# Performance work log

Hardware: AMD Instinct MI355X
Metric: run time of the kernel (lower is better)

Reference implementation:

```python
import jax, jax.numpy as jnp
import numpy as np
from jax import lax

# --- Haar (db1) wavelet filters, per WTConv (dec filters use reversed pywt taps) ---
_R = 0.7071067811865476
_lo = jnp.array([_R, _R], jnp.float32)
_hi = jnp.array([_R, -_R], jnp.float32)
# order: LL, (hi rows)x(lo cols), (lo rows)x(hi cols), HH  — matches WTConv stack order
DEC = jnp.stack([_lo[:, None] * _lo[None, :], _hi[:, None] * _lo[None, :],
                 _lo[:, None] * _hi[None, :], _hi[:, None] * _hi[None, :]])  # [4,2,2]
REC = DEC  # Haar is orthogonal: rec filters equal dec filters


def dwconv(x, w):
    # depthwise conv, SAME padding; x [b,c,h,w], w [c,1,kh,kw]
    return lax.conv_general_dilated(x, w, (1, 1), 'SAME',
                                    feature_group_count=x.shape[1],
                                    dimension_numbers=('NCHW', 'OIHW', 'NCHW'))


def wtconv(x, base_w, base_s, wav_w, wav_s):
    # WTConv2d, wt_levels=1, Haar: base depthwise path + wavelet-domain depthwise conv path
    b, c, h, w = x.shape
    # analysis: stride-2 2x2 filters == non-overlapping block contraction
    s = jnp.einsum('bchpwq,fpq->bcfhw', x.reshape(b, c, h // 2, 2, w // 2, 2), DEC)
    s = s.reshape(b, 4 * c, h // 2, w // 2)
    s = dwconv(s, wav_w) * wav_s[None, :, None, None]  # conv subbands + scale (init 0.1)
    # synthesis: transposed stride-2 conv == block expansion
    y = jnp.einsum('bcfhw,fpq->bchpwq', s.reshape(b, c, 4, h // 2, w // 2), REC)
    y = y.reshape(b, c, h, w)
    return dwconv(x, base_w) * base_s[None, :, None, None] + y


def _forward(x, crossFeat, Wq, Wk, Wv, temperature,
             qdw_base_w, qdw_base_s, qdw_wav_w, qdw_wav_s,
             kdw_base_w, kdw_base_s, kdw_wav_w, kdw_wav_s,
             vdw_base_w, vdw_base_s, vdw_wav_w, vdw_wav_s,
             proj_base_w, proj_base_s, proj_wav_w, proj_wav_s):
    heads = temperature.shape[0]
    b, _, H, W = crossFeat.shape
    q = jnp.einsum('bchw,oc->bohw', x, Wq)          # 1x1 conv, bias=False
    k = jnp.einsum('bchw,oc->bohw', crossFeat, Wk)
    v = jnp.einsum('bchw,oc->bohw', crossFeat, Wv)
    q = wtconv(q, qdw_base_w, qdw_base_s, qdw_wav_w, qdw_wav_s)
    k = wtconv(k, kdw_base_w, kdw_base_s, kdw_wav_w, kdw_wav_s)
    v = wtconv(v, vdw_base_w, vdw_base_s, vdw_wav_w, vdw_wav_s)
    dim = q.shape[1]
    # F.interpolate(mode='bilinear', align_corners=False) == jax.image.resize 'bilinear'
    q = jax.image.resize(q, (b, dim, H, W), 'bilinear')
    ch = dim // heads
    q = q.reshape(b, heads, ch, H * W)
    k = k.reshape(b, heads, ch, H * W)
    v = v.reshape(b, heads, ch, H * W)
    # L2-normalize along spatial dim (torch F.normalize eps=1e-12)
    q = q / jnp.maximum(jnp.linalg.norm(q, axis=-1, keepdims=True), 1e-12)
    k = k / jnp.maximum(jnp.linalg.norm(k, axis=-1, keepdims=True), 1e-12)
    attn = jnp.einsum('bhcn,bhdn->bhcd', q, k) * temperature[None]  # [b,h,ch,ch]
    attn = jax.nn.softmax(attn, axis=-1)
    out = jnp.einsum('bhcd,bhdn->bhcn', attn, v).reshape(b, dim, H, W)
    return wtconv(out, proj_base_w, proj_base_s, proj_wav_w, proj_wav_s)


def setup_inputs() -> dict:
    key = jax.random.key(0)
    ks = iter(jax.random.split(key, 32))
    B, CIN, DIM, HEADS = 2, 256, 256, 8
    d = {}
    d['x'] = jax.random.normal(next(ks), (B, CIN, 64, 64), jnp.float32)
    d['crossFeat'] = jax.random.normal(next(ks), (B, CIN, 128, 128), jnp.float32)
    d['Wq'] = jax.random.normal(next(ks), (DIM, CIN), jnp.float32) * 0.05
    d['Wk'] = jax.random.normal(next(ks), (DIM, CIN), jnp.float32) * 0.05
    d['Wv'] = jax.random.normal(next(ks), (DIM, CIN), jnp.float32) * 0.05
    d['temperature'] = jnp.ones((HEADS, 1, 1), jnp.float32)
    for pre, ksz in [('qdw', 3), ('kdw', 3), ('vdw', 3), ('proj', 1)]:
        d[pre + '_base_w'] = jax.random.normal(next(ks), (DIM, 1, ksz, ksz), jnp.float32) * 0.1
        d[pre + '_base_s'] = jnp.ones((DIM,), jnp.float32)
        d[pre + '_wav_w'] = jax.random.normal(next(ks), (4 * DIM, 1, ksz, ksz), jnp.float32) * 0.1
        d[pre + '_wav_s'] = 0.1 * jnp.ones((4 * DIM,), jnp.float32)
    return d


def reference(x, crossFeat, Wq, Wk, Wv, temperature,
              qdw_base_w, qdw_base_s, qdw_wav_w, qdw_wav_s,
              kdw_base_w, kdw_base_s, kdw_wav_w, kdw_wav_s,
              vdw_base_w, vdw_base_s, vdw_wav_w, vdw_wav_s,
              proj_base_w, proj_base_s, proj_wav_w, proj_wav_s):
    return _forward(x, crossFeat, Wq, Wk, Wv, temperature,
                    qdw_base_w, qdw_base_s, qdw_wav_w, qdw_wav_s,
                    kdw_base_w, kdw_base_s, kdw_wav_w, kdw_wav_s,
                    vdw_base_w, vdw_base_s, vdw_wav_w, vdw_wav_s,
                    proj_base_w, proj_base_s, proj_wav_w, proj_wav_s)
```

## Files before the change

### kernel.cpp

```cpp
#include <hip/hip_runtime.h>
#include <math.h>

constexpr int B_ = 2;
constexpr int C_ = 256;
constexpr int Hb_ = 128, Wb_ = 128;
constexpr int Nb_ = Hb_ * Wb_;
constexpr int Hs_ = 64, Ws_ = 64;
constexpr int Ns_ = Hs_ * Ws_;
constexpr int HEADS_ = 8;
constexpr int CHD_ = C_ / HEADS_;

typedef float f32x4 __attribute__((ext_vector_type(4)));
typedef short bf16x8 __attribute__((ext_vector_type(8)));
typedef unsigned short u16x8 __attribute__((ext_vector_type(8)));

__device__ inline void cvt_split(float f, unsigned short& h, unsigned short& l) {
  unsigned u = __float_as_uint(f);
  unsigned r = u + 0x7fffu + ((u >> 16) & 1u);
  h = (unsigned short)(r >> 16);
  float hf = __uint_as_float((unsigned)h << 16);
  float lo = f - hf;
  unsigned u2 = __float_as_uint(lo);
  unsigned r2 = u2 + 0x7fffu + ((u2 >> 16) & 1u);
  l = (unsigned short)(r2 >> 16);
}

__global__ __launch_bounds__(256) void cvt_split_T(const float* __restrict__ X,
                                                   unsigned short* __restrict__ Xh,
                                                   unsigned short* __restrict__ Xl,
                                                   int NTOT) {
  __shared__ float xs[64][72];
  const int b  = blockIdx.z;
  const int c0 = blockIdx.y * 64;
  const int n0 = blockIdx.x * 64;
  const int t  = threadIdx.x;
  const float* xb = X + ((size_t)(b * C_ + c0)) * NTOT + n0;
  {
    int cl = t >> 4, n4 = (t & 15) << 2;
#pragma unroll
    for (int i = 0; i < 4; ++i) {
      float4 v = *(const float4*)(xb + (size_t)(cl + 16 * i) * NTOT + n4);
      *(float4*)&xs[cl + 16 * i][n4] = v;
    }
  }
  __syncthreads();
  const int n_l = t >> 2, cqb = t & 3;
  size_t obase = ((size_t)b * NTOT + n0 + n_l) * C_ + c0;
#pragma unroll
  for (int it = 0; it < 2; ++it) {
    int cq = it * 4 + cqb;
    u16x8 hv, lv;
#pragma unroll
    for (int j = 0; j < 8; ++j) {
      unsigned short h, l;
      cvt_split(xs[cq * 8 + j][n_l], h, l);
      hv[j] = h; lv[j] = l;
    }
    *(u16x8*)(Xh + obase + cq * 8) = hv;
    *(u16x8*)(Xl + obase + cq * 8) = lv;
  }
}

__global__ void cvt_w(const float* __restrict__ Wq, const float* __restrict__ Wk,
                      const float* __restrict__ Wv, unsigned short* __restrict__ Wp) {
  int i = blockIdx.x * 256 + threadIdx.x;
  int m = i >> 16, idx = i & 65535;
  const float* src = (m == 0) ? Wq : (m == 1) ? Wk : Wv;
  unsigned short h, l;
  cvt_split(src[idx], h, l);
  Wp[(size_t)m * 131072 + idx] = h;
  Wp[(size_t)m * 131072 + 65536 + idx] = l;
}

template<bool DUAL>
__global__ __launch_bounds__(256) void gemm_mfma(
    const unsigned short* __restrict__ XhT, const unsigned short* __restrict__ XlT,
    const unsigned short* __restrict__ Wh1, const unsigned short* __restrict__ Wl1,
    const unsigned short* __restrict__ Wh2, const unsigned short* __restrict__ Wl2,
    float* __restrict__ out1, float* __restrict__ out2, int NTOT) {
  __shared__ __align__(16) unsigned short XhL[64][40];
  __shared__ __align__(16) unsigned short XlL[64][40];
  const int b  = blockIdx.z;
  const int o0 = blockIdx.y * 64;
  const int n0 = blockIdx.x * 64;
  const int t  = threadIdx.x;
  const int w = t >> 6, lane = t & 63;
  const int lr = lane & 15, lk = lane >> 4;
  const unsigned short* xh = XhT + ((size_t)b * NTOT + n0) * C_;
  const unsigned short* xl = XlT + ((size_t)b * NTOT + n0) * C_;
  const int arow = o0 + w * 16 + lr;
  f32x4 acc1[4] = {};
  f32x4 acc2[4] = {};
  const int sn = t >> 2, scq = (t & 3) << 3;
  for (int c0 = 0; c0 < C_; c0 += 32) {
    {
      size_t off = (size_t)sn * C_ + c0 + scq;
      *(u16x8*)&XhL[sn][scq] = *(const u16x8*)(xh + off);
      *(u16x8*)&XlL[sn][scq] = *(const u16x8*)(xl + off);
    }
    size_t aoff = (size_t)arow * C_ + c0 + lk * 8;
    bf16x8 a1h = *(const bf16x8*)(Wh1 + aoff);
    bf16x8 a1l = *(const bf16x8*)(Wl1 + aoff);
    bf16x8 a2h, a2l;
    if constexpr (DUAL) {
      a2h = *(const bf16x8*)(Wh2 + aoff);
      a2l = *(const bf16x8*)(Wl2 + aoff);
    }
    __syncthreads();
#pragma unroll
    for (int s = 0; s < 4; ++s) {
      bf16x8 bh = *(const bf16x8*)&XhL[s * 16 + lr][lk * 8];
      bf16x8 bl = *(const bf16x8*)&XlL[s * 16 + lr][lk * 8];
      acc1[s] = __builtin_amdgcn_mfma_f32_16x16x32_bf16(a1h, bh, acc1[s], 0, 0, 0);
      acc1[s] = __builtin_amdgcn_mfma_f32_16x16x32_bf16(a1h, bl, acc1[s], 0, 0, 0);
      acc1[s] = __builtin_amdgcn_mfma_f32_16x16x32_bf16(a1l, bh, acc1[s], 0, 0, 0);
      if constexpr (DUAL) {
        acc2[s] = __builtin_amdgcn_mfma_f32_16x16x32_bf16(a2h, bh, acc2[s], 0, 0, 0);
        acc2[s] = __builtin_amdgcn_mfma_f32_16x16x32_bf16(a2h, bl, acc2[s], 0, 0, 0);
        acc2[s] = __builtin_amdgcn_mfma_f32_16x16x32_bf16(a2l, bh, acc2[s], 0, 0, 0);
      }
    }
    __syncthreads();
  }
  float* o1 = out1 + ((size_t)(b * C_ + o0 + w * 16)) * NTOT + n0;
#pragma unroll
  for (int s = 0; s < 4; ++s)
#pragma unroll
    for (int r = 0; r < 4; ++r)
      o1[(size_t)(lk * 4 + r) * NTOT + s * 16 + lr] = acc1[s][r];
  if constexpr (DUAL) {
    float* o2 = out2 + ((size_t)(b * C_ + o0 + w * 16)) * NTOT + n0;
#pragma unroll
    for (int s = 0; s < 4; ++s)
#pragma unroll
      for (int r = 0; r < 4; ++r)
        o2[(size_t)(lk * 4 + r) * NTOT + s * 16 + lr] = acc2[s][r];
  }
}

template<int HP>
__global__ __launch_bounds__(256) void wtconv_fused(
    const float* __restrict__ x, const float* __restrict__ bw,
    const float* __restrict__ bs, const float* __restrict__ ww,
    const float* __restrict__ wsc, float* __restrict__ out,
    float* __restrict__ nrm) {
  constexpr int NT = HP / 64;
  const int tile = blockIdx.x;
  const int c = blockIdx.y, b = blockIdx.z;
  const int oy = (tile / NT) * 64, ox = (tile % NT) * 64;
  const float* xp = x + ((size_t)(b * C_) + c) * HP * HP;

  __shared__ float xt[68][76];
  __shared__ f32x4 sb4[34][36];
  __shared__ float red[4];

  float wb[9];
#pragma unroll
  for (int i = 0; i < 9; ++i) wb[i] = bw[c * 9 + i];
  const float sbase = bs[c];
  f32x4 wv4[9]; f32x4 sv4;
#pragma unroll
  for (int i = 0; i < 9; ++i) {
    wv4[i].x = ww[(c * 4 + 0) * 9 + i];
    wv4[i].y = ww[(c * 4 + 1) * 9 + i];
    wv4[i].z = ww[(c * 4 + 2) * 9 + i];
    wv4[i].w = ww[(c * 4 + 3) * 9 + i];
  }
  sv4.x = wsc[c * 4 + 0]; sv4.y = wsc[c * 4 + 1];
  sv4.z = wsc[c * 4 + 2]; sv4.w = wsc[c * 4 + 3];

  const int t = threadIdx.x;
  for (int p = t; p < 68 * 18; p += 256) {
    int r = p / 18, k4 = (p % 18) << 2;
    int gy = oy - 2 + r, gx = ox - 4 + k4;
    float4 v = make_float4(0.f, 0.f, 0.f, 0.f);
    if ((unsigned)gy < (unsigned)HP && (unsigned)gx < (unsigned)HP)
      v = *(const float4*)(xp + (size_t)gy * HP + gx);
    *(float4*)&xt[r][k4] = v;
  }
  __syncthreads();
  for (int p = t; p < 34 * 34; p += 256) {
    int i = p / 34, j = p % 34;
    float p00 = xt[2 * i][2 * j + 2],     p01 = xt[2 * i][2 * j + 3];
    float p10 = xt[2 * i + 1][2 * j + 2], p11 = xt[2 * i + 1][2 * j + 3];
    f32x4 s;
    s.x = 0.5f * (p00 + p01 + p10 + p11);
    s.y = 0.5f * (p00 + p01 - p10 - p11);
    s.z = 0.5f * (p00 - p01 + p10 - p11);
    s.w = 0.5f * (p00 - p01 - p10 + p11);
    sb4[i][j] = s;
  }
  __syncthreads();

  float nacc = 0.f;
  float* op0 = out + ((size_t)(b * C_) + c) * HP * HP;
  for (int p = t; p < 32 * 32; p += 256) {
    int i = p >> 5, j = p & 31;
    f32x4 a4 = {0.f, 0.f, 0.f, 0.f};
#pragma unroll
    for (int dh = 0; dh < 3; ++dh)
#pragma unroll
      for (int dw = 0; dw < 3; ++dw)
        a4 += sb4[i + dh][j + dw] * wv4[dh * 3 + dw];
    f32x4 s4 = a4 * sv4;
    float pp[4][4];
#pragma unroll
    for (int r = 0; r < 4; ++r)
#pragma unroll
      for (int cc = 0; cc < 4; ++cc)
        pp[r][cc] = xt[2 * i + 1 + r][2 * j + 3 + cc];
    float o4[2][2];
#pragma unroll
    for (int di = 0; di < 2; ++di)
#pragma unroll
      for (int dj = 0; dj < 2; ++dj) {
        float a = 0.f;
#pragma unroll
        for (int dh = 0; dh < 3; ++dh)
#pragma unroll
          for (int dw = 0; dw < 3; ++dw)
            a = fmaf(pp[di + dh][dj + dw], wb[dh * 3 + dw], a);
        a *= sbase;
        float s1 = di ? -s4.y : s4.y;
        float s2 = dj ? -s4.z : s4.z;
        float s3 = (di ^ dj) ? -s4.w : s4.w;
        o4[di][dj] = a + 0.5f * (s4.x + s1 + s2 + s3);
      }
    float* op = op0 + (size_t)(oy + 2 * i) * HP + ox + 2 * j;
    *(float2*)op        = make_float2(o4[0][0], o4[0][1]);
    *(float2*)(op + HP) = make_float2(o4[1][0], o4[1][1]);
    nacc += o4[0][0] * o4[0][0] + o4[0][1] * o4[0][1] +
            o4[1][0] * o4[1][0] + o4[1][1] * o4[1][1];
  }
  if (nrm != nullptr) {
#pragma unroll
    for (int m = 32; m; m >>= 1) nacc += __shfl_xor(nacc, m, 64);
    int lane = t & 63, wv_ = t >> 6;
    if (lane == 0) red[wv_] = nacc;
    __syncthreads();
    if (t == 0)
      atomicAdd(&nrm[b * C_ + c], red[0] + red[1] + red[2] + red[3]);
  }
}

__global__ __launch_bounds__(256) void resize2x_norm(const float* __restrict__ in,
                                                     float* __restrict__ out,
                                                     float* __restrict__ rnq_sum) {
  const int bc = blockIdx.x;
  const int t = threadIdx.x;
  __shared__ float xs[64][65];
  __shared__ float red[4];
  const float* ip = in + (size_t)bc * Ns_;
  for (int p = t; p < 1024; p += 256) {
    float4 v = *(const float4*)&ip[p << 2];
    int r = p >> 4, c0 = (p & 15) << 2;
    xs[r][c0] = v.x; xs[r][c0 + 1] = v.y; xs[r][c0 + 2] = v.z; xs[r][c0 + 3] = v.w;
  }
  __syncthreads();
  float* op = out + (size_t)bc * Nb_;
  float nacc = 0.f;
#pragma unroll
  for (int it = 0; it < 16; ++it) {
    int p = t + it * 256;
    int i = p >> 5;
    int jc = p & 31;
    int ti = i >> 1; bool oi = i & 1;
    int r0 = oi ? ti : (ti > 0 ? ti - 1 : 0);
    int r1 = oi ? (ti < 63 ? ti + 1 : 63) : ti;
    float wr0 = oi ? 0.75f : 0.25f, wr1 = oi ? 0.25f : 0.75f;
    int cb = jc << 1;
    int cm1 = cb > 0 ? cb - 1 : 0;
    int cp2 = cb < 62 ? cb + 2 : 63;
    float a0 = xs[r0][cm1], a1 = xs[r0][cb], a2 = xs[r0][cb + 1], a3 = xs[r0][cp2];
    float b0 = xs[r1][cm1], b1 = xs[r1][cb], b2 = xs[r1][cb + 1], b3 = xs[r1][cp2];
    float ha0 = 0.25f * a0 + 0.75f * a1, hb0 = 0.25f * b0 + 0.75f * b1;
    float ha1 = 0.75f * a1 + 0.25f * a2, hb1 = 0.75f * b1 + 0.25f * b2;
    float ha2 = 0.25f * a1 + 0.75f * a2, hb2 = 0.25f * b1 + 0.75f * b2;
    float ha3 = 0.75f * a2 + 0.25f * a3, hb3 = 0.75f * b2 + 0.25f * b3;
    float4 o = make_float4(wr0 * ha0 + wr1 * hb0, wr0 * ha1 + wr1 * hb1,
                           wr0 * ha2 + wr1 * hb2, wr0 * ha3 + wr1 * hb3);
    *(float4*)&op[p << 2] = o;
    nacc += o.x * o.x + o.y * o.y + o.z * o.z + o.w * o.w;
  }
#pragma unroll
  for (int m = 32; m; m >>= 1) nacc += __shfl_xor(nacc, m, 64);
  int lane = t & 63, wv = t >> 6;
  if (lane == 0) red[wv] = nacc;
  __syncthreads();
  if (t == 0) rnq_sum[bc] = red[0] + red[1] + red[2] + red[3];
}

__global__ void zero_buf(float* __restrict__ p, int n) {
  int i = blockIdx.x * blockDim.x + threadIdx.x;
  if (i < n) p[i] = 0.f;
}

__global__ __launch_bounds__(256) void gram_qk(const float* __restrict__ q,
                                               const float* __restrict__ k,
                                               float* __restrict__ gram) {
  const int b = blockIdx.z, h = blockIdx.y, sl = blockIdx.x;
  constexpr int NS = Nb_ / 32;
  const int n0 = sl * NS;
  const int t = threadIdx.x;
  const int tc = t >> 4, td = t & 15;
  const float* qb = q + ((size_t)b * C_ + h * CHD_) * Nb_;
  const float* kb = k + ((size_t)b * C_ + h * CHD_) * Nb_;
  __shared__ float qs[32][132];
  __shared__ float kst[128][34];
  float a00 = 0.f, a01 = 0.f, a10 = 0.f, a11 = 0.f;
  for (int nc = 0; nc < NS; nc += 128) {
    for (int i = t; i < 1024; i += 256) {
      int row = i >> 5, nc4 = (i & 31) << 2;
      float4 qv = *(const float4*)&qb[(size_t)row * Nb_ + n0 + nc + nc4];
      *(float4*)&qs[row][nc4] = qv;
      float4 kv = *(const float4*)&kb[(size_t)row * Nb_ + n0 + nc + nc4];
      kst[nc4 + 0][row] = kv.x; kst[nc4 + 1][row] = kv.y;
      kst[nc4 + 2][row] = kv.z; kst[nc4 + 3][row] = kv.w;
    }
    __syncthreads();
#pragma unroll 8
    for (int nn = 0; nn < 128; ++nn) {
      float q0 = qs[2 * tc][nn], q1 = qs[2 * tc + 1][nn];
      float2 kk = *(float2*)&kst[nn][2 * td];
      a00 = fmaf(q0, kk.x, a00); a01 = fmaf(q0, kk.y, a01);
      a10 = fmaf(q1, kk.x, a10); a11 = fmaf(q1, kk.y, a11);
    }
    __syncthreads();
  }
  float* gp = gram + ((size_t)(b * HEADS_ + h) * CHD_ + 2 * tc) * CHD_ + 2 * td;
  atomicAdd(&gp[0], a00);
  atomicAdd(&gp[1], a01);
  atomicAdd(&gp[CHD_], a10);
  atomicAdd(&gp[CHD_ + 1], a11);
}

__global__ __launch_bounds__(1024) void attn_softmax(const float* __restrict__ gram,
                                                     const float* __restrict__ rnq_sum,
                                                     const float* __restrict__ rnk_sum,
                                                     const float* __restrict__ temp,
                                                     float* __restrict__ attn) {
  const int h = blockIdx.x, b = blockIdx.y;
  const int t = threadIdx.x;
  const int c = t >> 5, d = t & 31;
  size_t gi = ((size_t)(b * HEADS_ + h) * CHD_ + c) * CHD_ + d;
  float rq = 1.f / fmaxf(sqrtf(rnq_sum[b * C_ + h * CHD_ + c]), 1e-12f);
  float rk = 1.f / fmaxf(sqrtf(rnk_sum[b * C_ + h * CHD_ + d]), 1e-12f);
  float val = gram[gi] * rq * rk * temp[h];
  float m = val;
#pragma unroll
  for (int s = 16; s; s >>= 1) m = fmaxf(m, __shfl_xor(m, s, 64));
  float e = expf(val - m);
  float ssum = e;
#pragma unroll
  for (int s = 16; s; s >>= 1) ssum += __shfl_xor(ssum, s, 64);
  attn[gi] = e / ssum;
}

__global__ __launch_bounds__(256) void av_proj(const float* __restrict__ attn,
                                               const float* __restrict__ v,
                                               const float* __restrict__ p_bw,
                                               const float* __restrict__ p_bs,
                                               const float* __restrict__ p_ww,
                                               const float* __restrict__ p_ws,
                                               float* __restrict__ out) {
  const int bh = blockIdx.y;
  const int b = bh >> 3, h = bh & 7;
  const int half = threadIdx.x >> 7;
  const int pl = threadIdx.x & 127;
  const int p = blockIdx.x * 128 + pl;
  const int bi = p >> 6, bj = p & 63;
  __shared__ float at[32][36];
  for (int i = threadIdx.x; i < 1024; i += 256)
    at[i & 31][i >> 5] = attn[(size_t)bh * 1024 + i];
  __syncthreads();
  const float* vb = v + ((size_t)b * C_ + h * CHD_) * Nb_;
  const int n00 = (2 * bi) * Wb_ + 2 * bj;
  float acc[16][4] = {};
  for (int d = 0; d < 32; ++d) {
    const float* vp = vb + (size_t)d * Nb_ + n00;
    float2 vt = *(const float2*)vp;
    float2 vbt = *(const float2*)(vp + Wb_);
    float4 a0 = *(float4*)&at[d][half * 16];
    float4 a1 = *(float4*)&at[d][half * 16 + 4];
    float4 a2 = *(float4*)&at[d][half * 16 + 8];
    float4 a3 = *(float4*)&at[d][half * 16 + 12];
    float av[16] = {a0.x, a0.y, a0.z, a0.w, a1.x, a1.y, a1.z, a1.w,
                    a2.x, a2.y, a2.z, a2.w, a3.x, a3.y, a3.z, a3.w};
#pragma unroll
    for (int cc = 0; cc < 16; ++cc) {
      acc[cc][0] = fmaf(av[cc], vt.x,  acc[cc][0]);
      acc[cc][1] = fmaf(av[cc], vt.y,  acc[cc][1]);
      acc[cc][2] = fmaf(av[cc], vbt.x, acc[cc][2]);
      acc[cc][3] = fmaf(av[cc], vbt.y, acc[cc][3]);
    }
  }
  float* ob = out + ((size_t)b * C_ + h * CHD_) * Nb_;
#pragma unroll
  for (int cc = 0; cc < 16; ++cc) {
    int lc = half * 16 + cc;
    int gc = h * CHD_ + lc;
    float p00 = acc[cc][0], p01 = acc[cc][1], p10 = acc[cc][2], p11 = acc[cc][3];
    float ll = 0.5f * (p00 + p01 + p10 + p11) * (p_ww[gc * 4 + 0] * p_ws[gc * 4 + 0]);
    float hl = 0.5f * (p00 + p01 - p10 - p11) * (p_ww[gc * 4 + 1] * p_ws[gc * 4 + 1]);
    float lh = 0.5f * (p00 - p01 + p10 - p11) * (p_ww[gc * 4 + 2] * p_ws[gc * 4 + 2]);
    float hh = 0.5f * (p00 - p01 - p10 + p11) * (p_ww[gc * 4 + 3] * p_ws[gc * 4 + 3]);
    float bb = p_bw[gc] * p_bs[gc];
    float* op = ob + (size_t)lc * Nb_ + n00;
    *(float2*)op         = make_float2(p00 * bb + 0.5f * (ll + hl + lh + hh),
                                       p01 * bb + 0.5f * (ll + hl - lh - hh));
    *(float2*)(op + Wb_) = make_float2(p10 * bb + 0.5f * (ll - hl + lh - hh),
                                       p11 * bb + 0.5f * (ll - hl - lh + hh));
  }
}

extern "C" void kernel_launch(void* const* d_in, const int* in_sizes, int n_in,
                              void* d_out, int out_size, void* d_ws, size_t ws_size,
                              hipStream_t stream) {
  const float* x    = (const float*)d_in[0];
  const float* cf   = (const float*)d_in[1];
  const float* Wq   = (const float*)d_in[2];
  const float* Wk   = (const float*)d_in[3];
  const float* Wv   = (const float*)d_in[4];
  const float* temp = (const float*)d_in[5];
  const float* q_bw = (const float*)d_in[6];
  const float* q_bs = (const float*)d_in[7];
  const float* q_ww = (const float*)d_in[8];
  const float* q_ws = (const float*)d_in[9];
  const float* k_bw = (const float*)d_in[10];
  const float* k_bs = (const float*)d_in[11];
  const float* k_ww = (const float*)d_in[12];
  const float* k_ws = (const float*)d_in[13];
  const float* v_bw = (const float*)d_in[14];
  const float* v_bs = (const float*)d_in[15];
  const float* v_ww = (const float*)d_in[16];
  const float* v_ws = (const float*)d_in[17];
  const float* p_bw = (const float*)d_in[18];
  const float* p_bs = (const float*)d_in[19];
  const float* p_ww = (const float*)d_in[20];
  const float* p_ws = (const float*)d_in[21];

  float* ws   = (float*)d_ws;
  float* A    = ws;
  float* Bb   = A  + 2097152;
  float* Cb   = Bb + 8388608;
  float* Fb   = Cb + 8388608;
  float* Gb   = Fb + 2097152;
  float* Hb   = Gb + 8388608;
  float* XhKf = Hb + 8388608;
  float* XlKf = XhKf + 4194304;
  float* Xhxf = XlKf + 4194304;
  float* Xlxf = Xhxf + 1048576;
  float* Wpf  = Xlxf + 1048576;
  float* rnq  = Wpf + 196608;
  float* rnk  = rnq + 512;
  float* gram = rnk + 512;
  float* attn = gram + 16384;
  unsigned short* XhK = (unsigned short*)XhKf;
  unsigned short* XlK = (unsigned short*)XlKf;
  unsigned short* Xhx = (unsigned short*)Xhxf;
  unsigned short* Xlx = (unsigned short*)Xlxf;
  unsigned short* Wp  = (unsigned short*)Wpf;

  zero_buf<<<(16896 + 255) / 256, 256, 0, stream>>>(rnk, 16896);

  cvt_split_T<<<dim3(Nb_ / 64, C_ / 64, B_), 256, 0, stream>>>(cf, XhK, XlK, Nb_);
  cvt_split_T<<<dim3(Ns_ / 64, C_ / 64, B_), 256, 0, stream>>>(x,  Xhx, Xlx, Ns_);
  cvt_w<<<3 * 65536 / 256, 256, 0, stream>>>(Wq, Wk, Wv, Wp);

  gemm_mfma<false><<<dim3(Ns_ / 64, C_ / 64, B_), 256, 0, stream>>>(
      Xhx, Xlx, Wp, Wp + 65536, nullptr, nullptr, A, nullptr, Ns_);
  gemm_mfma<true><<<dim3(Nb_ / 64, C_ / 64, B_), 256, 0, stream>>>(
      XhK, XlK, Wp + 131072, Wp + 196608, Wp + 262144, Wp + 327680, Bb, Cb, Nb_);

  wtconv_fused<64><<<dim3(1, C_, B_), 256, 0, stream>>>(A, q_bw, q_bs, q_ww, q_ws, Fb, nullptr);
  wtconv_fused<128><<<dim3(4, C_, B_), 256, 0, stream>>>(Bb, k_bw, k_bs, k_ww, k_ws, Gb, rnk);
  wtconv_fused<128><<<dim3(4, C_, B_), 256, 0, stream>>>(Cb, v_bw, v_bs, v_ww, v_ws, Hb, nullptr);

  resize2x_norm<<<B_ * C_, 256, 0, stream>>>(Fb, Bb, rnq);

  gram_qk<<<dim3(32, HEADS_, B_), 256, 0, stream>>>(Bb, Gb, gram);
  attn_softmax<<<dim3(HEADS_, B_), 1024, 0, stream>>>(gram, rnq, rnk, temp, attn);

  av_proj<<<dim3(Nb_ / 4 / 128, B_ * HEADS_), 256, 0, stream>>>(
      attn, Hb, p_bw, p_bs, p_ww, p_ws, (float*)d_out);
}
```

Baseline: 286.6 us.

## Double-buffer GEMM tiles with register prefetch and widen N tile to 128

The split-bf16 MFMA projection GEMM now uses a 128-column N tile instead of 64 and double-buffers the X tiles in shared memory. Global loads for the next K-step are issued into registers before the current step's MFMAs, which removes one barrier per iteration and hides load latency. Weight fragments are also prefetched one step ahead. In exchange the kernel uses more accumulator registers and shared memory, and half as many blocks are launched, which may lower occupancy. The shared layout loses its padding, so LDS bank conflicts are possible.

```diff
diff --git a/kernel.cpp b/kernel.cpp
--- a/kernel.cpp
+++ b/kernel.cpp
@@ -78,39 +78,56 @@
     const unsigned short* __restrict__ Wh1, const unsigned short* __restrict__ Wl1,
     const unsigned short* __restrict__ Wh2, const unsigned short* __restrict__ Wl2,
     float* __restrict__ out1, float* __restrict__ out2, int NTOT) {
-  __shared__ __align__(16) unsigned short XhL[64][40];
-  __shared__ __align__(16) unsigned short XlL[64][40];
+  __shared__ __align__(16) unsigned short XhL[2][128 * 32];
+  __shared__ __align__(16) unsigned short XlL[2][128 * 32];
   const int b  = blockIdx.z;
   const int o0 = blockIdx.y * 64;
-  const int n0 = blockIdx.x * 64;
+  const int n0 = blockIdx.x * 128;
   const int t  = threadIdx.x;
   const int w = t >> 6, lane = t & 63;
   const int lr = lane & 15, lk = lane >> 4;
   const unsigned short* xh = XhT + ((size_t)b * NTOT + n0) * C_;
   const unsigned short* xl = XlT + ((size_t)b * NTOT + n0) * C_;
   const int arow = o0 + w * 16 + lr;
-  f32x4 acc1[4] = {};
-  f32x4 acc2[4] = {};
-  const int sn = t >> 2, scq = (t & 3) << 3;
-  for (int c0 = 0; c0 < C_; c0 += 32) {
-    {
-      size_t off = (size_t)sn * C_ + c0 + scq;
-      *(u16x8*)&XhL[sn][scq] = *(const u16x8*)(xh + off);
-      *(u16x8*)&XlL[sn][scq] = *(const u16x8*)(xl + off);
-    }
-    size_t aoff = (size_t)arow * C_ + c0 + lk * 8;
-    bf16x8 a1h = *(const bf16x8*)(Wh1 + aoff);
-    bf16x8 a1l = *(const bf16x8*)(Wl1 + aoff);
-    bf16x8 a2h, a2l;
-    if constexpr (DUAL) {
-      a2h = *(const bf16x8*)(Wh2 + aoff);
-      a2l = *(const bf16x8*)(Wl2 + aoff);
-    }
-    __syncthreads();
-#pragma unroll
-    for (int s = 0; s < 4; ++s) {
-      bf16x8 bh = *(const bf16x8*)&XhL[s * 16 + lr][lk * 8];
-      bf16x8 bl = *(const bf16x8*)&XlL[s * 16 + lr][lk * 8];
+  const size_t abase = (size_t)arow * C_ + lk * 8;
+  const size_t g0 = (size_t)(t >> 2) * C_ + (size_t)(t & 3) * 8;
+  const size_t g1 = (size_t)((t >> 2) + 64) * C_ + (size_t)(t & 3) * 8;
+  f32x4 acc1[8] = {};
+  f32x4 acc2[8] = {};
+  *(u16x8*)&XhL[0][t * 8]         = *(const u16x8*)(xh + g0);
+  *(u16x8*)&XhL[0][(t + 256) * 8] = *(const u16x8*)(xh + g1);
+  *(u16x8*)&XlL[0][t * 8]         = *(const u16x8*)(xl + g0);
+  *(u16x8*)&XlL[0][(t + 256) * 8] = *(const u16x8*)(xl + g1);
+  bf16x8 a1h = *(const bf16x8*)(Wh1 + abase);
+  bf16x8 a1l = *(const bf16x8*)(Wl1 + abase);
+  bf16x8 a2h = {}, a2l = {};
+  if constexpr (DUAL) {
+    a2h = *(const bf16x8*)(Wh2 + abase);
+    a2l = *(const bf16x8*)(Wl2 + abase);
+  }
+  __syncthreads();
+  for (int step = 0; step < 8; ++step) {
+    const int cur = step & 1;
+    u16x8 xr0h, xr1h, xr0l, xr1l;
+    bf16x8 n1h = {}, n1l = {}, n2h = {}, n2l = {};
+    const int c1 = (step + 1) * 32;
+    if (step < 7) {
+      xr0h = *(const u16x8*)(xh + g0 + c1);
+      xr1h = *(const u16x8*)(xh + g1 + c1);
+      xr0l = *(const u16x8*)(xl + g0 + c1);
+      xr1l = *(const u16x8*)(xl + g1 + c1);
+      n1h = *(const bf16x8*)(Wh1 + abase + c1);
+      n1l = *(const bf16x8*)(Wl1 + abase + c1);
+      if constexpr (DUAL) {
+        n2h = *(const bf16x8*)(Wh2 + abase + c1);
+        n2l = *(const bf16x8*)(Wl2 + abase + c1);
+      }
+    }
+#pragma unroll
+    for (int s = 0; s < 8; ++s) {
+      const int bo = ((s * 16 + lr) * 4 + lk) * 8;
+      bf16x8 bh = *(const bf16x8*)&XhL[cur][bo];
+      bf16x8 bl = *(const bf16x8*)&XlL[cur][bo];
       acc1[s] = __builtin_amdgcn_mfma_f32_16x16x32_bf16(a1h, bh, acc1[s], 0, 0, 0);
       acc1[s] = __builtin_amdgcn_mfma_f32_16x16x32_bf16(a1h, bl, acc1[s], 0, 0, 0);
       acc1[s] = __builtin_amdgcn_mfma_f32_16x16x32_bf16(a1l, bh, acc1[s], 0, 0, 0);
@@ -120,18 +137,27 @@
         acc2[s] = __builtin_amdgcn_mfma_f32_16x16x32_bf16(a2l, bh, acc2[s], 0, 0, 0);
       }
     }
+    if (step < 7) {
+      const int nxt = cur ^ 1;
+      *(u16x8*)&XhL[nxt][t * 8]         = xr0h;
+      *(u16x8*)&XhL[nxt][(t + 256) * 8] = xr1h;
+      *(u16x8*)&XlL[nxt][t * 8]         = xr0l;
+      *(u16x8*)&XlL[nxt][(t + 256) * 8] = xr1l;
+      a1h = n1h; a1l = n1l;
+      if constexpr (DUAL) { a2h = n2h; a2l = n2l; }
+    }
     __syncthreads();
   }
   float* o1 = out1 + ((size_t)(b * C_ + o0 + w * 16)) * NTOT + n0;
 #pragma unroll
-  for (int s = 0; s < 4; ++s)
+  for (int s = 0; s < 8; ++s)
 #pragma unroll
     for (int r = 0; r < 4; ++r)
       o1[(size_t)(lk * 4 + r) * NTOT + s * 16 + lr] = acc1[s][r];
   if constexpr (DUAL) {
     float* o2 = out2 + ((size_t)(b * C_ + o0 + w * 16)) * NTOT + n0;
 #pragma unroll
-    for (int s = 0; s < 4; ++s)
+    for (int s = 0; s < 8; ++s)
 #pragma unroll
       for (int r = 0; r < 4; ++r)
         o2[(size_t)(lk * 4 + r) * NTOT + s * 16 + lr] = acc2[s][r];
@@ -467,9 +493,9 @@
   cvt_split_T<<<dim3(Ns_ / 64, C_ / 64, B_), 256, 0, stream>>>(x,  Xhx, Xlx, Ns_);
   cvt_w<<<3 * 65536 / 256, 256, 0, stream>>>(Wq, Wk, Wv, Wp);
 
-  gemm_mfma<false><<<dim3(Ns_ / 64, C_ / 64, B_), 256, 0, stream>>>(
+  gemm_mfma<false><<<dim3(Ns_ / 128, C_ / 64, B_), 256, 0, stream>>>(
       Xhx, Xlx, Wp, Wp + 65536, nullptr, nullptr, A, nullptr, Ns_);
-  gemm_mfma<true><<<dim3(Nb_ / 64, C_ / 64, B_), 256, 0, stream>>>(
+  gemm_mfma<true><<<dim3(Nb_ / 128, C_ / 64, B_), 256, 0, stream>>>(
       XhK, XlK, Wp + 131072, Wp + 196608, Wp + 262144, Wp + 327680, Bb, Cb, Nb_);
 
   wtconv_fused<64><<<dim3(1, C_, B_), 256, 0, stream>>>(A, q_bw, q_bs, q_ww, q_ws, Fb, nullptr);
```

After: 280.3 us. 1.02x faster.
